# Optimization experiments

Measured on AMD Instinct MI355X. Metric: run time of the kernel, lower is better.

The kernel has to match this reference:

```python
import jax, jax.numpy as jnp
import numpy as np

NUM_EMBEDDINGS = 1024
EMBEDDING_DIM = 256
COMMITMENT_COST = 0.02


def setup_inputs() -> dict:
    key = jax.random.key(0)
    k1, k2 = jax.random.split(key)
    z = jax.random.normal(k1, (64, 256, 32, 32), dtype=jnp.float32)
    # torch init: uniform(-1/K, 1/K)
    emb = jax.random.uniform(k2, (NUM_EMBEDDINGS, EMBEDDING_DIM), dtype=jnp.float32,
                             minval=-1.0 / NUM_EMBEDDINGS, maxval=1.0 / NUM_EMBEDDINGS)
    return {"z": z, "emb": emb}


def reference(z, emb):
    n, d, h, w = z.shape
    # (N, D, H, W) -> (N*H*W, D)
    z_flat = jnp.transpose(z, (0, 2, 3, 1)).reshape(-1, d)
    # squared L2 distances: ||z||^2 - 2 z.E^T + ||E||^2  -> (NHW, K)
    distances = (jnp.sum(z_flat * z_flat, axis=1, keepdims=True)
                 - 2.0 * z_flat @ emb.T
                 + jnp.sum(emb * emb, axis=1))
    indices = jnp.argmin(distances, axis=1)  # (NHW,)
    z_q = jnp.transpose(emb[indices].reshape(n, h, w, d), (0, 3, 1, 2))  # (N, D, H, W)
    # straight-through estimator
    z_q_st = z + jax.lax.stop_gradient(z_q - z)
    commitment_loss = COMMITMENT_COST * jnp.mean((jax.lax.stop_gradient(z) - z_q) ** 2)
    codebook_loss = jnp.mean((z - jax.lax.stop_gradient(z_q)) ** 2)
    vq_loss = commitment_loss + codebook_loss
    indices_reshaped = indices.reshape(n, h, w)
    return z_q_st, indices_reshaped, vq_loss
```

## Files before the change

### kernel.cpp

```cpp
#include <hip/hip_runtime.h>
#include <hip/hip_bf16.h>
#include <float.h>

#define OUT_IDX_OFF 16777216
#define OUT_LOSS_OFF 16842752
#define CAND_OFF 8388608
#define GMIN_OFF 12582912
#define GCNT_OFF 13107200
#define NSLOT 32
#define DELTA 2.0e-3f

typedef __attribute__((ext_vector_type(8))) short short8;
typedef __attribute__((ext_vector_type(4))) float f32x4;

static __device__ __forceinline__ unsigned short f2bf(float f) {
  union { __hip_bfloat16 h; unsigned short u; } cv;
  cv.h = __float2bfloat16(f);
  return cv.u;
}

__global__ __launch_bounds__(256) void k_prep(const float* __restrict__ emb,
                                              unsigned short* __restrict__ E2,
                                              float* __restrict__ cws,
                                              int* __restrict__ gmin,
                                              int* __restrict__ gcnt,
                                              float* __restrict__ out) {
  const int k = blockIdx.x, d = threadIdx.x;
  const int tid = (k << 8) + d;
  if (tid < 65536) {
    gmin[tid] = 0x7f7f7f7f;
    gcnt[tid] = 0;
  }
  if (tid == 0) out[OUT_LOSS_OFF] = 0.0f;
  const float v = emb[k * 256 + d];
  __shared__ float red[256];
  __shared__ unsigned short row[256];
  row[d] = f2bf(v);
  red[d] = v * v;
  __syncthreads();
  for (int s = 128; s > 0; s >>= 1) {
    if (d < s) red[d] += red[d + s];
    __syncthreads();
  }
  if (d == 0) cws[k] = red[0];
  if (d < 32) ((short8*)&E2[k * 256])[d] = ((short8*)row)[d];
}

__global__ __launch_bounds__(256) void k_cvt4(const float* __restrict__ z,
                                              unsigned short* __restrict__ A2,
                                              float* __restrict__ aws) {
#pragma clang fp contract(off)
  __shared__ float tile[64][65];
  __shared__ float red2[128];
  const int t = threadIdx.x;
  const int p0 = blockIdx.x << 6;
  const int n = p0 >> 10, hw0 = p0 & 1023;
  const float* zb = z + (size_t)n * 262144 + hw0;
  const int hwl = (t & 15) << 2;
  const int dlb = t >> 4;
  const int row = t & 63, h = (t >> 6) & 1;
  const int pl = t >> 2, c = t & 3;

  float4 v[4];
#pragma unroll
  for (int i = 0; i < 4; ++i)
    v[i] = *(const float4*)&zb[(size_t)(dlb + i * 16) * 1024 + hwl];

  float acc[8];

  for (int dt = 0; dt < 4; ++dt) {
    if (dt) __syncthreads();
#pragma unroll
    for (int i = 0; i < 4; ++i) {
      const int dl = dlb + i * 16;
      tile[hwl + 0][dl] = v[i].x;
      tile[hwl + 1][dl] = v[i].y;
      tile[hwl + 2][dl] = v[i].z;
      tile[hwl + 3][dl] = v[i].w;
    }
    __syncthreads();
    if (dt < 3) {
      const float* zb2 = zb + (size_t)(dt + 1) * 65536;
#pragma unroll
      for (int i = 0; i < 4; ++i)
        v[i] = *(const float4*)&zb2[(size_t)(dlb + i * 16) * 1024 + hwl];
    }
    unsigned short* dst = &A2[(size_t)(p0 + pl) * 256 + dt * 64];
#pragma unroll
    for (int hh = 0; hh < 2; ++hh) {
      const int ch = c + hh * 4;
      unsigned short tmp[8];
#pragma unroll
      for (int j = 0; j < 8; ++j) tmp[j] = f2bf(tile[pl][ch * 8 + j]);
      *(short8*)&dst[ch * 8] = *(short8*)tmp;
    }
    if (t < 128 && (dt >> 1) == h) {
      if ((dt & 1) == 0) {
#pragma unroll
        for (int j = 0; j < 8; ++j) {
          const float x = tile[row][j];
          acc[j] = x * x;
        }
        for (int g = 1; g < 8; ++g)
#pragma unroll
          for (int j = 0; j < 8; ++j) {
            const float x = tile[row][g * 8 + j];
            const float p = x * x;
            acc[j] = acc[j] + p;
          }
      } else {
        for (int g = 8; g < 16; ++g)
#pragma unroll
          for (int j = 0; j < 8; ++j) {
            const float x = tile[row][(g - 8) * 8 + j];
            const float p = x * x;
            acc[j] = acc[j] + p;
          }
      }
    }
  }
  if (t < 128) {
    const float s = ((acc[0] + acc[1]) + (acc[2] + acc[3])) +
                    ((acc[4] + acc[5]) + (acc[6] + acc[7]));
    red2[t] = s;
  }
  __syncthreads();
  if (t < 64) aws[p0 + t] = red2[t] + red2[t + 64];
}

__global__ __launch_bounds__(256, 4) void k_gemm9(
    const unsigned short* __restrict__ A2, const unsigned short* __restrict__ E2,
    const float* __restrict__ cws, const float* __restrict__ aws,
    int* __restrict__ gmin, int* __restrict__ gcnt,
    float2* __restrict__ gcand) {
  __shared__ __align__(16) unsigned short As[128 * 64];
  __shared__ __align__(16) unsigned short Bs[128 * 64];
  __shared__ float a_l[128], c_l[128], rmkt[256], bmin[128];

  const int t = threadIdx.x;
  const int lane = t & 63;
  const int wave = __builtin_amdgcn_readfirstlane(t >> 6);
  const int wr = wave >> 1, wc = wave & 1;
  const int quad = lane >> 4, l15 = lane & 15;
  const int swa = l15 & 7;

  const int bid = blockIdx.x;
  const int L = ((bid & 7) << 9) + (bid >> 3);
  const int rb = L >> 3, ck = L & 7;
  const int r0 = rb << 7, k0 = ck << 7;

  if (t < 128) {
    a_l[t] = aws[r0 + t];
    c_l[t] = cws[k0 + t];
  }

  const int srow = t >> 3;
  const int gpos = t & 7;

  f32x4 acc[4][4];
#pragma unroll
  for (int a = 0; a < 4; ++a)
#pragma unroll
    for (int b = 0; b < 4; ++b) acc[a][b] = (f32x4)(0.0f);

  for (int kt = 0; kt < 4; ++kt) {
    if (kt) __syncthreads();
#pragma unroll
    for (int i = 0; i < 4; ++i) {
      const int row = (i << 5) + srow;
      const int gsrc = gpos ^ (row & 7);
      const unsigned short* sa =
          A2 + (((size_t)(r0 + row)) << 8) + (kt << 6) + (gsrc << 3);
      __builtin_amdgcn_global_load_lds(
          (const __attribute__((address_space(1))) void*)sa,
          (__attribute__((address_space(3))) void*)(As + (i << 11) +
                                                    (wave << 9)),
          16, 0, 0);
      const unsigned short* sb =
          E2 + (((size_t)(k0 + row)) << 8) + (kt << 6) + (gsrc << 3);
      __builtin_amdgcn_global_load_lds(
          (const __attribute__((address_space(1))) void*)sb,
          (__attribute__((address_space(3))) void*)(Bs + (i << 11) +
                                                    (wave << 9)),
          16, 0, 0);
    }
    __syncthreads();
#pragma unroll
    for (int ks = 0; ks < 2; ++ks) {
      short8 af[4], bf[4];
#pragma unroll
      for (int tr = 0; tr < 4; ++tr)
        af[tr] = *(const short8*)&As[(wr * 64 + tr * 16 + l15) * 64 +
                                     (((ks * 4 + quad) ^ swa) << 3)];
#pragma unroll
      for (int tc = 0; tc < 4; ++tc)
        bf[tc] = *(const short8*)&Bs[(wc * 64 + tc * 16 + l15) * 64 +
                                     (((ks * 4 + quad) ^ swa) << 3)];
#pragma unroll
      for (int tr = 0; tr < 4; ++tr)
#pragma unroll
        for (int tc = 0; tc < 4; ++tc)
          acc[tr][tc] = __builtin_amdgcn_mfma_f32_16x16x32_bf16(
              af[tr], bf[tc], acc[tr][tc], 0, 0, 0);
    }
  }

#pragma unroll
  for (int tr = 0; tr < 4; ++tr)
#pragma unroll
    for (int rg = 0; rg < 4; ++rg) {
      const int rloc = wr * 64 + tr * 16 + quad * 4 + rg;
      const float av = a_l[rloc];
      float mn = FLT_MAX;
#pragma unroll
      for (int tc = 0; tc < 4; ++tc) {
        const int cloc = wc * 64 + tc * 16 + l15;
        const float s = av + fmaf(-2.0f, acc[tr][tc][rg], c_l[cloc]);
        mn = fminf(mn, s);
      }
      mn = fminf(mn, __shfl_xor(mn, 1));
      mn = fminf(mn, __shfl_xor(mn, 2));
      mn = fminf(mn, __shfl_xor(mn, 4));
      mn = fminf(mn, __shfl_xor(mn, 8));
      if (l15 == 0) rmkt[rloc * 2 + wc] = mn;
    }
  __syncthreads();
  if (t < 128) {
    const float m = fminf(rmkt[t * 2], rmkt[t * 2 + 1]);
    const int old = atomicMin(&gmin[r0 + t], __float_as_int(m));
    bmin[t] = fminf(m, __int_as_float(old));
  }
  __syncthreads();
#pragma unroll
  for (int tr = 0; tr < 4; ++tr)
#pragma unroll
    for (int rg = 0; rg < 4; ++rg) {
      const int rloc = wr * 64 + tr * 16 + quad * 4 + rg;
      const float av = a_l[rloc];
      const float lim = bmin[rloc] + DELTA;
#pragma unroll
      for (int tc = 0; tc < 4; ++tc) {
        const int cloc = wc * 64 + tc * 16 + l15;
        const float s = av + fmaf(-2.0f, acc[tr][tc][rg], c_l[cloc]);
        if (s <= lim) {
          const int pos = atomicAdd(&gcnt[r0 + rloc], 1);
          if (pos < NSLOT)
            gcand[(size_t)(r0 + rloc) * NSLOT + pos] =
                make_float2(s, __int_as_float(k0 + cloc));
        }
      }
    }
}

__global__ __launch_bounds__(256) void k_finish2(
    const float* __restrict__ z, const float* __restrict__ emb,
    const float* __restrict__ cws, const float* __restrict__ aws,
    const int* __restrict__ gmin, const int* __restrict__ gcnt,
    const float2* __restrict__ gcand, int* __restrict__ idxws,
    float* __restrict__ out, int write_zq) {
  const int r = (blockIdx.x << 8) + threadIdx.x;
  const float lim = __int_as_float(gmin[r]) + DELTA;
  int m = gcnt[r];
  if (m > NSLOT) m = NSLOT;
  const int n = r >> 10, hw = r & 1023;
  const float* zp = z + (size_t)n * 262144 + hw;
  const float a = aws[r];
  float bestv = FLT_MAX;
  int besti = 0x7fffffff;
  for (int ci = 0; ci < m; ++ci) {
    const float2 p = gcand[(size_t)r * NSLOT + ci];
    if (p.x > lim) continue;
    const int k = __float_as_int(p.y);
    const float* ep = emb + (size_t)k * 256;
    float dot = 0.0f;
#pragma unroll 8
    for (int d = 0; d < 256; ++d) dot = fmaf(zp[(size_t)d * 1024], ep[d], dot);
    float s = fmaf(-2.0f, dot, a);
    s = s + cws[k];
    if (s < bestv || (s == bestv && k < besti)) {
      bestv = s;
      besti = k;
    }
  }
  out[OUT_IDX_OFF + r] = (float)besti;
  if (write_zq) {
    float* ob = out + (size_t)n * 262144 + hw;
    const float4* e4 = (const float4*)(emb + (size_t)besti * 256);
#pragma unroll 4
    for (int d0 = 0; d0 < 64; ++d0) {
      const float4 e = e4[d0];
      ob[(size_t)(d0 * 4 + 0) * 1024] = e.x;
      ob[(size_t)(d0 * 4 + 1) * 1024] = e.y;
      ob[(size_t)(d0 * 4 + 2) * 1024] = e.z;
      ob[(size_t)(d0 * 4 + 3) * 1024] = e.w;
    }
  } else {
    idxws[r] = besti;
  }
  float c = bestv;
#pragma unroll
  for (int off = 1; off < 64; off <<= 1) c += __shfl_xor(c, off);
  if ((threadIdx.x & 63) == 0)
    atomicAdd(&out[OUT_LOSS_OFF], c * (1.02f / 16777216.0f));
}

__global__ __launch_bounds__(256) void k_out2(const float* __restrict__ emb,
                                              const int* __restrict__ idxws,
                                              float* __restrict__ out) {
  __shared__ float zq[32][257];
  __shared__ int sidx[32];
  const int t = threadIdx.x;
  const int p0 = blockIdx.x << 5;
  const int n = p0 >> 10, hw0 = p0 & 1023;
  if (t < 32) sidx[t] = idxws[p0 + t];
  __syncthreads();
#pragma unroll
  for (int it = 0; it < 8; ++it) {
    const int i = t + (it << 8);
    const int p = i >> 6;
    const int q = (i & 63) << 2;
    const float4 v = *(const float4*)&emb[(size_t)sidx[p] * 256 + q];
    zq[p][q] = v.x;
    zq[p][q + 1] = v.y;
    zq[p][q + 2] = v.z;
    zq[p][q + 3] = v.w;
  }
  __syncthreads();
  const int p = t & 31, d0 = t >> 5;
  float* ob = out + (size_t)n * 262144 + hw0 + p;
#pragma unroll
  for (int dd = 0; dd < 32; ++dd) {
    const int d = (dd << 3) + d0;
    ob[(size_t)d * 1024] = zq[p][d];
  }
}

extern "C" void kernel_launch(void* const* d_in, const int* in_sizes, int n_in,
                              void* d_out, int out_size, void* d_ws,
                              size_t ws_size, hipStream_t stream) {
  const float* z = (const float*)d_in[0];
  const float* emb = (const float*)d_in[1];
  float* out = (float*)d_out;

  unsigned short* E2 = (unsigned short*)d_ws;
  float* cws = (float*)(E2 + 262144);
  float* aws = cws + 1024;
  int* idxws = (int*)(aws + 65536);
  unsigned short* A2 = (unsigned short*)d_out;

  const size_t WS_NEED = 1052672u + 262144u + 262144u + 16777216u;
  const int big_ws = (ws_size >= WS_NEED) ? 1 : 0;
  int* gmin;
  int* gcnt;
  float2* gcand;
  if (big_ws) {
    gmin = idxws + 65536;
    gcnt = gmin + 65536;
    gcand = (float2*)(gcnt + 65536);
  } else {
    gcand = (float2*)(out + CAND_OFF);
    gmin = (int*)(out + GMIN_OFF);
    gcnt = (int*)(out + GCNT_OFF);
  }

  k_prep<<<dim3(1024), dim3(256), 0, stream>>>(emb, E2, cws, gmin, gcnt, out);
  k_cvt4<<<dim3(1024), dim3(256), 0, stream>>>(z, A2, aws);
  k_gemm9<<<dim3(4096), dim3(256), 0, stream>>>(A2, E2, cws, aws, gmin, gcnt,
                                                gcand);
  k_finish2<<<dim3(256), dim3(256), 0, stream>>>(z, emb, cws, aws, gmin, gcnt,
                                                 gcand, idxws, out, big_ws);
  if (!big_ws)
    k_out2<<<dim3(2048), dim3(256), 0, stream>>>(emb, idxws, out);
}
```

Baseline: 347.0 us.

## Split candidate rescoring across four lanes per row with shared z tile

The finish kernel now stages a 256x64 tile of z in shared memory with coalesced float4 loads, assigns four threads per row to rescore candidates in parallel, and reduces the best index with shuffles. The z_q write is restructured so consecutive threads write consecutive pixels. The grid grows from 256 to 1024 blocks. The aim is to remove the long serial per-thread candidate loop and its strided z reads, which left few blocks and poor coalescing. The cost is 64KB of shared memory per block, which limits occupancy.

```diff
diff --git a/kernel.cpp b/kernel.cpp
--- a/kernel.cpp
+++ b/kernel.cpp
@@ -252,29 +252,48 @@
     }
 }
 
-__global__ __launch_bounds__(256) void k_finish2(
+__global__ __launch_bounds__(256) void k_finish3(
     const float* __restrict__ z, const float* __restrict__ emb,
     const float* __restrict__ cws, const float* __restrict__ aws,
     const int* __restrict__ gmin, const int* __restrict__ gcnt,
     const float2* __restrict__ gcand, int* __restrict__ idxws,
     float* __restrict__ out, int write_zq) {
-  const int r = (blockIdx.x << 8) + threadIdx.x;
+  __shared__ float ztile[256][64];
+  __shared__ int sidx[64];
+  const int t = threadIdx.x;
+  const int p0 = blockIdx.x << 6;
+  const int n = p0 >> 10, hw0 = p0 & 1023;
+  const float* zb = z + (size_t)n * 262144 + hw0;
+
+  const int hwl = (t & 15) << 2;
+  const int dl = t >> 4;
+#pragma unroll
+  for (int i = 0; i < 16; ++i) {
+    const int d = dl + (i << 4);
+    const float4 v = *(const float4*)&zb[(size_t)d * 1024 + hwl];
+    ztile[d][hwl + 0] = v.x;
+    ztile[d][hwl + 1] = v.y;
+    ztile[d][hwl + 2] = v.z;
+    ztile[d][hwl + 3] = v.w;
+  }
+  __syncthreads();
+
+  const int pl = t >> 2, sub = t & 3;
+  const int r = p0 + pl;
   const float lim = __int_as_float(gmin[r]) + DELTA;
   int m = gcnt[r];
   if (m > NSLOT) m = NSLOT;
-  const int n = r >> 10, hw = r & 1023;
-  const float* zp = z + (size_t)n * 262144 + hw;
   const float a = aws[r];
   float bestv = FLT_MAX;
   int besti = 0x7fffffff;
-  for (int ci = 0; ci < m; ++ci) {
+  for (int ci = sub; ci < m; ci += 4) {
     const float2 p = gcand[(size_t)r * NSLOT + ci];
     if (p.x > lim) continue;
     const int k = __float_as_int(p.y);
     const float* ep = emb + (size_t)k * 256;
     float dot = 0.0f;
 #pragma unroll 8
-    for (int d = 0; d < 256; ++d) dot = fmaf(zp[(size_t)d * 1024], ep[d], dot);
+    for (int d = 0; d < 256; ++d) dot = fmaf(ztile[d][pl], ep[d], dot);
     float s = fmaf(-2.0f, dot, a);
     s = s + cws[k];
     if (s < bestv || (s == bestv && k < besti)) {
@@ -282,26 +301,34 @@
       besti = k;
     }
   }
-  out[OUT_IDX_OFF + r] = (float)besti;
+#pragma unroll
+  for (int off = 1; off < 4; off <<= 1) {
+    const float ov = __shfl_xor(bestv, off);
+    const int oi = __shfl_xor(besti, off);
+    if (ov < bestv || (ov == bestv && oi < besti)) {
+      bestv = ov;
+      besti = oi;
+    }
+  }
+  if (sub == 0) {
+    out[OUT_IDX_OFF + r] = (float)besti;
+    sidx[pl] = besti;
+    if (!write_zq) idxws[r] = besti;
+  }
+  float c = (sub == 0) ? bestv : 0.0f;
+#pragma unroll
+  for (int off = 1; off < 64; off <<= 1) c += __shfl_xor(c, off);
+  if ((t & 63) == 0)
+    atomicAdd(&out[OUT_LOSS_OFF], c * (1.02f / 16777216.0f));
+
   if (write_zq) {
-    float* ob = out + (size_t)n * 262144 + hw;
-    const float4* e4 = (const float4*)(emb + (size_t)besti * 256);
-#pragma unroll 4
-    for (int d0 = 0; d0 < 64; ++d0) {
-      const float4 e = e4[d0];
-      ob[(size_t)(d0 * 4 + 0) * 1024] = e.x;
-      ob[(size_t)(d0 * 4 + 1) * 1024] = e.y;
-      ob[(size_t)(d0 * 4 + 2) * 1024] = e.z;
-      ob[(size_t)(d0 * 4 + 3) * 1024] = e.w;
-    }
-  } else {
-    idxws[r] = besti;
-  }
-  float c = bestv;
-#pragma unroll
-  for (int off = 1; off < 64; off <<= 1) c += __shfl_xor(c, off);
-  if ((threadIdx.x & 63) == 0)
-    atomicAdd(&out[OUT_LOSS_OFF], c * (1.02f / 16777216.0f));
+    __syncthreads();
+    const int px = t & 63, dq = t >> 6;
+    const float* ep = emb + (size_t)sidx[px] * 256 + (dq << 6);
+    float* ob = out + (size_t)n * 262144 + ((size_t)(dq << 6)) * 1024 + hw0 + px;
+#pragma unroll 8
+    for (int i = 0; i < 64; ++i) ob[(size_t)i * 1024] = ep[i];
+  }
 }
 
 __global__ __launch_bounds__(256) void k_out2(const float* __restrict__ emb,
@@ -367,8 +394,8 @@
   k_cvt4<<<dim3(1024), dim3(256), 0, stream>>>(z, A2, aws);
   k_gemm9<<<dim3(4096), dim3(256), 0, stream>>>(A2, E2, cws, aws, gmin, gcnt,
                                                 gcand);
-  k_finish2<<<dim3(256), dim3(256), 0, stream>>>(z, emb, cws, aws, gmin, gcnt,
-                                                 gcand, idxws, out, big_ws);
+  k_finish3<<<dim3(1024), dim3(256), 0, stream>>>(z, emb, cws, aws, gmin, gcnt,
+                                                  gcand, idxws, out, big_ws);
   if (!big_ws)
     k_out2<<<dim3(2048), dim3(256), 0, stream>>>(emb, idxws, out);
 }
```

Result: faster. 296.1 us (-14.7%).
